# Kernel tuning notes

Hardware: AMD Instinct MI355X
Metric: run time of the kernel (lower is better)

Reference implementation:

```python
import jax, jax.numpy as jnp
import numpy as np

N = 8192        # nodes
E = 49152       # edges (~avg degree 6, triangular mesh)
H = 6           # GATv2 heads
C = 512         # hidden_size (per-head out channels)
F_IN = 2 + C    # GATv2 in_channels = coord(2) + hidden(512)
ALL_FEAT = 37   # deform_in_c-2 + 16 + 16
NUM_LOOP = 3
LRELU_SLOPE = 0.2


def setup_inputs() -> dict:
    key = jax.random.key(0)
    ks = jax.random.split(key, 10)
    x = jax.random.uniform(ks[0], (N, 7), dtype=jnp.float32)
    local_feat = jax.random.normal(ks[1], (N, 16), dtype=jnp.float32)
    conv_feat = jax.random.normal(ks[2], (N, 16), dtype=jnp.float32)
    edge_index = jax.random.randint(ks[3], (2, E), 0, N, dtype=jnp.int64)
    bd_mask = jnp.zeros((N,), jnp.int32)  # poly_mesh=False path
    W_lin = jax.random.normal(ks[4], (ALL_FEAT, C), dtype=jnp.float32) / np.float32(np.sqrt(ALL_FEAT))
    b_lin = jnp.zeros((C,), jnp.float32)
    Wl = jax.random.normal(ks[5], (F_IN, H * C), dtype=jnp.float32) / np.float32(np.sqrt(F_IN))
    Wr = jax.random.normal(ks[6], (F_IN, H * C), dtype=jnp.float32) / np.float32(np.sqrt(F_IN))
    att = jax.random.normal(ks[7], (H, C), dtype=jnp.float32) / np.float32(np.sqrt(C))
    gat_bias = jnp.zeros((C,), jnp.float32)
    W_coord = jax.random.normal(ks[8], (C, 2), dtype=jnp.float32) / np.float32(np.sqrt(C))
    b_coord = jnp.zeros((2,), jnp.float32)
    return dict(x=x, local_feat=local_feat, conv_feat=conv_feat,
                W_lin=W_lin, b_lin=b_lin, Wl=Wl, Wr=Wr, att=att,
                gat_bias=gat_bias, W_coord=W_coord, b_coord=b_coord,
                edge_index=edge_index, bd_mask=bd_mask)


def _gatv2(feat, src, dst, Wl, Wr, att, bias):
    # PyG GATv2Conv: lin_l on source, lin_r on target, additive attention
    n = feat.shape[0]
    xl = (feat @ Wl).reshape(n, H, C)            # source-side transform
    xr = (feat @ Wr).reshape(n, H, C)            # target-side transform
    e = xl[src] + xr[dst]                        # [E', H, C]
    e = jax.nn.leaky_relu(e, LRELU_SLOPE)
    logits = jnp.einsum('ehc,hc->eh', e, att)    # [E', H]
    m = jax.ops.segment_max(logits, dst, num_segments=n)
    m = jnp.where(jnp.isfinite(m), m, 0.0)
    a = jnp.exp(logits - m[dst])
    denom = jax.ops.segment_sum(a, dst, num_segments=n) + 1e-16
    alpha = a / denom[dst]                       # segment softmax over incoming edges
    msg = xl[src] * alpha[:, :, None]            # [E', H, C]
    out = jax.ops.segment_sum(msg, dst, num_segments=n)  # [N, H, C]
    return out.mean(axis=1) + bias               # concat=False -> mean over heads


def reference(x, local_feat, conv_feat, W_lin, b_lin, Wl, Wr, att, gat_bias,
              W_coord, b_coord, edge_index, bd_mask):
    coord = x[:, :2]
    hidden_in = jnp.concatenate([x[:, 2:], local_feat, conv_feat], axis=1)
    hidden = jax.nn.selu(hidden_in @ W_lin + b_lin)
    # GATv2Conv adds self-loops by default
    loops = jnp.arange(N, dtype=edge_index.dtype)
    src = jnp.concatenate([edge_index[0], loops])
    dst = jnp.concatenate([edge_index[1], loops])
    for _ in range(NUM_LOOP):
        up = coord[:, 0] == 1.0
        down = coord[:, 0] == 0.0
        left = coord[:, 1] == 0.0
        right = coord[:, 1] == 1.0
        feat = jnp.concatenate([coord, hidden], axis=1)   # [N, 514]
        hidden = jax.nn.selu(_gatv2(feat, src, dst, Wl, Wr, att, gat_bias))
        out = hidden @ W_coord + b_coord                  # [N, 2]
        ox = jnp.where(down, 0.0, jnp.where(up, 1.0, out[:, 0]))
        oy = jnp.where(right, 1.0, jnp.where(left, 0.0, out[:, 1]))
        coord = jnp.stack([ox, oy], axis=1)
    return coord
```

## Files before the change

kernel.cpp:

```cpp
#include <hip/hip_runtime.h>
#include <hip/hip_bf16.h>
#include <math.h>

#define N_NODES   8192
#define NUM_E     49152
#define NUM_EDGES (NUM_E + N_NODES)
#define H_HEADS   6
#define C_DIM     512
#define HC        (H_HEADS * C_DIM)
#define XLR       (2 * HC)
#define N_FEAT    37
#define LRELU_SLOPE 0.2f
#define SELU_LAMBDA 1.0507009873554805f
#define SELU_ALPHA  1.6732632423543772f

typedef __bf16 bf16_t;
typedef bf16_t bf16x8 __attribute__((ext_vector_type(8)));
typedef bf16_t bf16x4 __attribute__((ext_vector_type(4)));
typedef float  f32x4  __attribute__((ext_vector_type(4)));
typedef float  f32x2  __attribute__((ext_vector_type(2)));

__device__ __forceinline__ int edge_src(const int* ei, int e) {
    return e < NUM_E ? ei[e] : (e - NUM_E);
}
__device__ __forceinline__ int edge_dst(const int* ei, int e) {
    return e < NUM_E ? ei[NUM_E + e] : (e - NUM_E);
}
__device__ __forceinline__ float selu_f(float v) {
    return v > 0.f ? SELU_LAMBDA * v : SELU_LAMBDA * SELU_ALPHA * (__expf(v) - 1.f);
}
__device__ __forceinline__ void gload_lds16(const void* g, void* l) {
    __builtin_amdgcn_global_load_lds((const __attribute__((address_space(1))) void*)g,
                                     (__attribute__((address_space(3))) void*)l, 16, 0, 0);
}

__global__ __launch_bounds__(512) void k_hidden0(
    const float* __restrict__ x, const float* __restrict__ lf,
    const float* __restrict__ cf, const float* __restrict__ W,
    const float* __restrict__ b, bf16_t* __restrict__ hidden,
    float* __restrict__ coord)
{
    int n = blockIdx.x;
    int c = threadIdx.x;
    __shared__ float f[N_FEAT];
    if (c < 5)            f[c] = x[n*7 + 2 + c];
    else if (c < 21)      f[c] = lf[n*16 + (c-5)];
    else if (c < N_FEAT)  f[c] = cf[n*16 + (c-21)];
    if (c < 2) coord[n*2 + c] = x[n*7 + c];
    __syncthreads();
    float acc = b[c];
    #pragma unroll
    for (int k = 0; k < N_FEAT; ++k) acc = fmaf(f[k], W[k*C_DIM + c], acc);
    hidden[n*C_DIM + c] = (bf16_t)selu_f(acc);
}

__global__ __launch_bounds__(256) void k_wt_transpose(const float* __restrict__ W,
                                                      bf16_t* __restrict__ WT)
{
    __shared__ float tile[32][33];
    int k0 = blockIdx.y * 32;
    int n0 = blockIdx.x * 32;
    int tx = threadIdx.x & 31, ty = threadIdx.x >> 5;
    #pragma unroll
    for (int i = 0; i < 4; ++i)
        tile[ty + i*8][tx] = W[(size_t)(k0 + 2 + ty + i*8) * HC + n0 + tx];
    __syncthreads();
    #pragma unroll
    for (int i = 0; i < 4; ++i)
        WT[(size_t)(n0 + ty + i*8) * C_DIM + k0 + tx] = (bf16_t)tile[tx][ty + i*8];
}

__global__ void k_hist(const int* __restrict__ ei, int* __restrict__ counts) {
    int e = blockIdx.x * blockDim.x + threadIdx.x;
    if (e >= NUM_EDGES) return;
    atomicAdd(&counts[edge_dst(ei, e)], 1);
}

__global__ __launch_bounds__(256) void k_scan(const int* __restrict__ counts,
                                              int* __restrict__ row_ptr,
                                              int* __restrict__ cursor) {
    __shared__ int part[256];
    __shared__ int off[257];
    int t = threadIdx.x;
    int base = t * 32;
    int local[32];
    int s = 0;
    #pragma unroll
    for (int i = 0; i < 32; ++i) { local[i] = s; s += counts[base + i]; }
    part[t] = s;
    __syncthreads();
    if (t == 0) {
        off[0] = 0;
        for (int i = 0; i < 256; ++i) off[i+1] = off[i] + part[i];
    }
    __syncthreads();
    int o = off[t];
    #pragma unroll
    for (int i = 0; i < 32; ++i) {
        int v = o + local[i];
        row_ptr[base + i] = v;
        cursor[base + i]  = v;
    }
    if (t == 255) row_ptr[N_NODES] = off[256];
}

__global__ void k_scatter(const int* __restrict__ ei, int* __restrict__ cursor,
                          int* __restrict__ csr_src) {
    int e = blockIdx.x * blockDim.x + threadIdx.x;
    if (e >= NUM_EDGES) return;
    int pos = atomicAdd(&cursor[edge_dst(ei, e)], 1);
    csr_src[pos] = edge_src(ei, e);
}

#define GM 128
#define GN 128
#define GK 32
__global__ __launch_bounds__(256) void k_gemm_bf16(
    const bf16_t* __restrict__ A,
    const bf16_t* __restrict__ BT,
    const float*  __restrict__ Wl,
    const float*  __restrict__ Wr,
    const float*  __restrict__ coord,
    bf16_t* __restrict__ out)
{
    __shared__ bf16_t As[2][GM][GK];
    __shared__ bf16_t Bs[2][GM][GK];
    int tid  = threadIdx.x;
    int wave = tid >> 6;
    int lane = tid & 63;
    int rowBase = blockIdx.y * GM;
    int colBase = blockIdx.x * GN;
    int wr = (wave >> 1) * 64;
    int wc = (wave & 1) * 64;

    f32x4 acc[4][4] = {};

    int gsw = (((lane & 3) ^ ((lane >> 3) & 3))) * 8;
    const bf16_t* Ag = A  + (size_t)(rowBase + wave*32 + (lane >> 2)) * C_DIM + gsw;
    const bf16_t* Bg = BT + (size_t)(colBase + wave*32 + (lane >> 2)) * C_DIM + gsw;
    int m16 = lane & 15;
    int q8s = (((lane >> 4) ^ ((lane >> 1) & 3))) * 8;

    gload_lds16(Ag,            &As[0][wave*32     ][0]);
    gload_lds16(Ag + 16*C_DIM, &As[0][wave*32 + 16][0]);
    gload_lds16(Bg,            &Bs[0][wave*32     ][0]);
    gload_lds16(Bg + 16*C_DIM, &Bs[0][wave*32 + 16][0]);

    int p = 0;
    for (int k0 = 0; k0 < C_DIM; k0 += GK) {
        __syncthreads();
        if (k0 + GK < C_DIM) {
            gload_lds16(Ag + k0 + GK,            &As[p^1][wave*32     ][0]);
            gload_lds16(Ag + k0 + GK + 16*C_DIM, &As[p^1][wave*32 + 16][0]);
            gload_lds16(Bg + k0 + GK,            &Bs[p^1][wave*32     ][0]);
            gload_lds16(Bg + k0 + GK + 16*C_DIM, &Bs[p^1][wave*32 + 16][0]);
        }
        bf16x8 af[4], bfr[4];
        #pragma unroll
        for (int i = 0; i < 4; ++i) af[i]  = *(const bf16x8*)&As[p][wr + i*16 + m16][q8s];
        #pragma unroll
        for (int j = 0; j < 4; ++j) bfr[j] = *(const bf16x8*)&Bs[p][wc + j*16 + m16][q8s];
        #pragma unroll
        for (int i = 0; i < 4; ++i)
            #pragma unroll
            for (int j = 0; j < 4; ++j)
                acc[i][j] = __builtin_amdgcn_mfma_f32_16x16x32_bf16(bfr[j], af[i], acc[i][j], 0, 0, 0);
        p ^= 1;
    }

    const float* Wtop = (colBase < HC) ? Wl : Wr;
    int coff = (colBase < HC) ? 0 : HC;
    int q4 = (lane >> 4) * 4;

    float4 w0[4], w1[4];
    #pragma unroll
    for (int j = 0; j < 4; ++j) {
        int wcol = colBase + wc + j*16 + q4 - coff;
        w0[j] = *(const float4*)&Wtop[wcol];
        w1[j] = *(const float4*)&Wtop[HC + wcol];
    }
    #pragma unroll
    for (int i = 0; i < 4; ++i) {
        int row = rowBase + wr + i*16 + m16;
        float c0 = coord[row*2 + 0], c1 = coord[row*2 + 1];
        size_t rb = (size_t)row * XLR;
        #pragma unroll
        for (int j = 0; j < 4; ++j) {
            int col = colBase + wc + j*16 + q4;
            bf16x4 pk;
            pk[0] = (bf16_t)(acc[i][j][0] + c0 * w0[j].x + c1 * w1[j].x);
            pk[1] = (bf16_t)(acc[i][j][1] + c0 * w0[j].y + c1 * w1[j].y);
            pk[2] = (bf16_t)(acc[i][j][2] + c0 * w0[j].z + c1 * w1[j].z);
            pk[3] = (bf16_t)(acc[i][j][3] + c0 * w0[j].w + c1 * w1[j].w);
            *(bf16x4*)(out + rb + col) = pk;
        }
    }
}

#define MAX_DEG 128
__global__ __launch_bounds__(384) void k_attn_agg(
    const bf16_t* __restrict__ xlr,
    const int* __restrict__ row_ptr, const int* __restrict__ csr_src,
    const float* __restrict__ att,
    const float* __restrict__ gat_bias, const float* __restrict__ W_coord,
    const float* __restrict__ b_coord, const float* __restrict__ coord_in,
    bf16_t* __restrict__ hidden, float* __restrict__ coord_out)
{
    int n = blockIdx.x;
    int tid = threadIdx.x;
    int h = tid >> 6, lane = tid & 63;
    __shared__ int   s_src[MAX_DEG];
    __shared__ float s_acc[HC];
    __shared__ float s_red[12];

    int beg = row_ptr[n];
    int deg = min(row_ptr[n + 1] - beg, MAX_DEG);
    for (int j = tid; j < deg; j += 384) s_src[j] = csr_src[beg + j];
    __syncthreads();

    size_t off = (size_t)h * C_DIM + lane * 8;
    bf16x8 xrv = *(const bf16x8*)(xlr + (size_t)n * XLR + HC + off);
    f32x2 xr2[4], at2[4], ac2[4] = {};
    #pragma unroll
    for (int i = 0; i < 4; ++i) {
        xr2[i] = f32x2{(float)xrv[2*i], (float)xrv[2*i+1]};
        at2[i] = f32x2{att[off + 2*i], att[off + 2*i + 1]};
    }

    float l = 0.f;
    int j = 0;
    for (; j + 2 <= deg; j += 2) {
        bf16x8 xa = *(const bf16x8*)(xlr + (size_t)s_src[j]     * XLR + off);
        bf16x8 xb = *(const bf16x8*)(xlr + (size_t)s_src[j + 1] * XLR + off);
        f32x2 xla[4], xlb[4];
        #pragma unroll
        for (int i = 0; i < 4; ++i) {
            xla[i] = f32x2{(float)xa[2*i], (float)xa[2*i+1]};
            xlb[i] = f32x2{(float)xb[2*i], (float)xb[2*i+1]};
        }
        f32x2 sa = {0.f, 0.f}, sb = {0.f, 0.f};
        #pragma unroll
        for (int i = 0; i < 4; ++i) {
            f32x2 va = xla[i] + xr2[i];
            f32x2 vb = xlb[i] + xr2[i];
            sa += __builtin_elementwise_max(va, va * LRELU_SLOPE) * at2[i];
            sb += __builtin_elementwise_max(vb, vb * LRELU_SLOPE) * at2[i];
        }
        float suma = sa.x + sa.y, sumb = sb.x + sb.y;
        #pragma unroll
        for (int o = 1; o < 64; o <<= 1) {
            suma += __shfl_xor(suma, o);
            sumb += __shfl_xor(sumb, o);
        }
        float aa = __expf(suma), ab = __expf(sumb);
        l += aa + ab;
        #pragma unroll
        for (int i = 0; i < 4; ++i) ac2[i] += aa * xla[i] + ab * xlb[i];
    }
    if (j < deg) {
        bf16x8 xa = *(const bf16x8*)(xlr + (size_t)s_src[j] * XLR + off);
        f32x2 xla[4];
        #pragma unroll
        for (int i = 0; i < 4; ++i) xla[i] = f32x2{(float)xa[2*i], (float)xa[2*i+1]};
        f32x2 sa = {0.f, 0.f};
        #pragma unroll
        for (int i = 0; i < 4; ++i) {
            f32x2 va = xla[i] + xr2[i];
            sa += __builtin_elementwise_max(va, va * LRELU_SLOPE) * at2[i];
        }
        float suma = sa.x + sa.y;
        #pragma unroll
        for (int o = 1; o < 64; o <<= 1) suma += __shfl_xor(suma, o);
        float aa = __expf(suma);
        l += aa;
        #pragma unroll
        for (int i = 0; i < 4; ++i) ac2[i] += aa * xla[i];
    }

    float invl = 1.f / (l + 1e-16f) * (1.f / 6.f);
    #pragma unroll
    for (int i = 0; i < 4; ++i) {
        s_acc[off + 2*i]     = ac2[i].x * invl;
        s_acc[off + 2*i + 1] = ac2[i].y * invl;
    }
    __syncthreads();

    float p0 = 0.f, p1 = 0.f;
    for (int c = tid; c < C_DIM; c += 384) {
        float s = 0.f;
        #pragma unroll
        for (int hh = 0; hh < H_HEADS; ++hh) s += s_acc[hh * C_DIM + c];
        float hv = selu_f(s + gat_bias[c]);
        hidden[n * C_DIM + c] = (bf16_t)hv;
        p0 = fmaf(hv, W_coord[c * 2 + 0], p0);
        p1 = fmaf(hv, W_coord[c * 2 + 1], p1);
    }
    #pragma unroll
    for (int o = 32; o > 0; o >>= 1) { p0 += __shfl_down(p0, o); p1 += __shfl_down(p1, o); }
    if (lane == 0) { s_red[h * 2] = p0; s_red[h * 2 + 1] = p1; }
    __syncthreads();
    if (tid == 0) {
        float o0 = b_coord[0], o1 = b_coord[1];
        #pragma unroll
        for (int w = 0; w < H_HEADS; ++w) { o0 += s_red[w * 2]; o1 += s_red[w * 2 + 1]; }
        float cx = coord_in[n * 2 + 0], cy = coord_in[n * 2 + 1];
        float ox = (cx == 0.0f) ? 0.f : ((cx == 1.0f) ? 1.f : o0);
        float oy = (cy == 1.0f) ? 1.f : ((cy == 0.0f) ? 0.f : o1);
        coord_out[n * 2 + 0] = ox;
        coord_out[n * 2 + 1] = oy;
    }
}

extern "C" void kernel_launch(void* const* d_in, const int* in_sizes, int n_in,
                              void* d_out, int out_size, void* d_ws, size_t ws_size,
                              hipStream_t stream)
{
    const float* x       = (const float*)d_in[0];
    const float* lf      = (const float*)d_in[1];
    const float* cf      = (const float*)d_in[2];
    const float* W_lin   = (const float*)d_in[3];
    const float* b_lin   = (const float*)d_in[4];
    const float* Wl      = (const float*)d_in[5];
    const float* Wr      = (const float*)d_in[6];
    const float* att     = (const float*)d_in[7];
    const float* gbias   = (const float*)d_in[8];
    const float* W_coord = (const float*)d_in[9];
    const float* b_coord = (const float*)d_in[10];
    const int*   ei      = (const int*)d_in[11];

    char* w = (char*)d_ws;
    auto alloc = [&](size_t bytes) { char* p = w; w += (bytes + 255) & ~255ull; return p; };
    bf16_t*   hidden  = (bf16_t*)alloc((size_t)N_NODES * C_DIM * 2);
    bf16_t*   WT      = (bf16_t*)alloc((size_t)XLR * C_DIM * 2);
    bf16_t*   xlr     = (bf16_t*)alloc((size_t)N_NODES * XLR * 2);
    int*      counts  = (int*)alloc((size_t)N_NODES * 4);
    int*      row_ptr = (int*)alloc((size_t)(N_NODES + 1) * 4);
    int*      cursor  = (int*)alloc((size_t)N_NODES * 4);
    int*      csr_src = (int*)alloc((size_t)NUM_EDGES * 4);
    float*    cA      = (float*)alloc((size_t)N_NODES * 2 * 4);
    float*    cB      = (float*)alloc((size_t)N_NODES * 2 * 4);

    hipMemsetAsync(counts, 0, (size_t)N_NODES * 4, stream);
    k_hidden0<<<N_NODES, 512, 0, stream>>>(x, lf, cf, W_lin, b_lin, hidden, cA);
    {
        dim3 tg(HC / 32, C_DIM / 32);
        k_wt_transpose<<<tg, 256, 0, stream>>>(Wl, WT);
        k_wt_transpose<<<tg, 256, 0, stream>>>(Wr, WT + (size_t)HC * C_DIM);
    }
    k_hist<<<(NUM_EDGES + 255) / 256, 256, 0, stream>>>(ei, counts);
    k_scan<<<1, 256, 0, stream>>>(counts, row_ptr, cursor);
    k_scatter<<<(NUM_EDGES + 255) / 256, 256, 0, stream>>>(ei, cursor, csr_src);

    float* cin = cA;
    for (int it = 0; it < 3; ++it) {
        float* cout = (it == 2) ? (float*)d_out : ((it == 0) ? cB : cA);
        dim3 g(XLR / GN, N_NODES / GM);
        k_gemm_bf16<<<g, 256, 0, stream>>>(hidden, WT, Wl, Wr, cin, xlr);
        k_attn_agg<<<N_NODES, 384, 0, stream>>>(xlr, row_ptr, csr_src, att,
                                                gbias, W_coord, b_coord, cin, hidden, cout);
        cin = cout;
    }
}
```

Before: 603.5 us.

## Load GEMM fragments directly from global memory, dropping LDS staging

```diff
diff --git a/kernel.cpp b/kernel.cpp
--- a/kernel.cpp
+++ b/kernel.cpp
@@ -29,10 +29,6 @@
 __device__ __forceinline__ float selu_f(float v) {
     return v > 0.f ? SELU_LAMBDA * v : SELU_LAMBDA * SELU_ALPHA * (__expf(v) - 1.f);
 }
-__device__ __forceinline__ void gload_lds16(const void* g, void* l) {
-    __builtin_amdgcn_global_load_lds((const __attribute__((address_space(1))) void*)g,
-                                     (__attribute__((address_space(3))) void*)l, 16, 0, 0);
-}
 
 __global__ __launch_bounds__(512) void k_hidden0(
     const float* __restrict__ x, const float* __restrict__ lf,
@@ -114,7 +110,6 @@
 
 #define GM 128
 #define GN 128
-#define GK 32
 __global__ __launch_bounds__(256) void k_gemm_bf16(
     const bf16_t* __restrict__ A,
     const bf16_t* __restrict__ BT,
@@ -123,75 +118,59 @@
     const float*  __restrict__ coord,
     bf16_t* __restrict__ out)
 {
-    __shared__ bf16_t As[2][GM][GK];
-    __shared__ bf16_t Bs[2][GM][GK];
     int tid  = threadIdx.x;
     int wave = tid >> 6;
     int lane = tid & 63;
-    int rowBase = blockIdx.y * GM;
-    int colBase = blockIdx.x * GN;
-    int wr = (wave >> 1) * 64;
-    int wc = (wave & 1) * 64;
+    int rowBase = blockIdx.y * GM + (wave >> 1) * 64;
+    int colBase = blockIdx.x * GN + (wave & 1) * 64;
+    int m16 = lane & 15;
+    int q8  = (lane >> 4) * 8;
+
+    const bf16_t* Ap[4];
+    const bf16_t* Bp[4];
+    #pragma unroll
+    for (int i = 0; i < 4; ++i) {
+        Ap[i] = A  + (size_t)(rowBase + i*16 + m16) * C_DIM + q8;
+        Bp[i] = BT + (size_t)(colBase + i*16 + m16) * C_DIM + q8;
+    }
 
     f32x4 acc[4][4] = {};
 
-    int gsw = (((lane & 3) ^ ((lane >> 3) & 3))) * 8;
-    const bf16_t* Ag = A  + (size_t)(rowBase + wave*32 + (lane >> 2)) * C_DIM + gsw;
-    const bf16_t* Bg = BT + (size_t)(colBase + wave*32 + (lane >> 2)) * C_DIM + gsw;
-    int m16 = lane & 15;
-    int q8s = (((lane >> 4) ^ ((lane >> 1) & 3))) * 8;
-
-    gload_lds16(Ag,            &As[0][wave*32     ][0]);
-    gload_lds16(Ag + 16*C_DIM, &As[0][wave*32 + 16][0]);
-    gload_lds16(Bg,            &Bs[0][wave*32     ][0]);
-    gload_lds16(Bg + 16*C_DIM, &Bs[0][wave*32 + 16][0]);
-
-    int p = 0;
-    for (int k0 = 0; k0 < C_DIM; k0 += GK) {
-        __syncthreads();
-        if (k0 + GK < C_DIM) {
-            gload_lds16(Ag + k0 + GK,            &As[p^1][wave*32     ][0]);
-            gload_lds16(Ag + k0 + GK + 16*C_DIM, &As[p^1][wave*32 + 16][0]);
-            gload_lds16(Bg + k0 + GK,            &Bs[p^1][wave*32     ][0]);
-            gload_lds16(Bg + k0 + GK + 16*C_DIM, &Bs[p^1][wave*32 + 16][0]);
-        }
+    #pragma unroll 2
+    for (int k0 = 0; k0 < C_DIM; k0 += 32) {
         bf16x8 af[4], bfr[4];
         #pragma unroll
-        for (int i = 0; i < 4; ++i) af[i]  = *(const bf16x8*)&As[p][wr + i*16 + m16][q8s];
-        #pragma unroll
-        for (int j = 0; j < 4; ++j) bfr[j] = *(const bf16x8*)&Bs[p][wc + j*16 + m16][q8s];
+        for (int i = 0; i < 4; ++i) af[i]  = *(const bf16x8*)(Ap[i] + k0);
+        #pragma unroll
+        for (int j = 0; j < 4; ++j) bfr[j] = *(const bf16x8*)(Bp[j] + k0);
         #pragma unroll
         for (int i = 0; i < 4; ++i)
             #pragma unroll
             for (int j = 0; j < 4; ++j)
                 acc[i][j] = __builtin_amdgcn_mfma_f32_16x16x32_bf16(bfr[j], af[i], acc[i][j], 0, 0, 0);
-        p ^= 1;
-    }
-
-    const float* Wtop = (colBase < HC) ? Wl : Wr;
-    int coff = (colBase < HC) ? 0 : HC;
+    }
+
+    int colB0 = blockIdx.x * GN;
+    const float* Wtop = (colB0 < HC) ? Wl : Wr;
+    int coff = (colB0 < HC) ? 0 : HC;
     int q4 = (lane >> 4) * 4;
 
-    float4 w0[4], w1[4];
-    #pragma unroll
-    for (int j = 0; j < 4; ++j) {
-        int wcol = colBase + wc + j*16 + q4 - coff;
-        w0[j] = *(const float4*)&Wtop[wcol];
-        w1[j] = *(const float4*)&Wtop[HC + wcol];
-    }
     #pragma unroll
     for (int i = 0; i < 4; ++i) {
-        int row = rowBase + wr + i*16 + m16;
+        int row = rowBase + i*16 + m16;
         float c0 = coord[row*2 + 0], c1 = coord[row*2 + 1];
         size_t rb = (size_t)row * XLR;
         #pragma unroll
         for (int j = 0; j < 4; ++j) {
-            int col = colBase + wc + j*16 + q4;
+            int col = colBase + j*16 + q4;
+            int wcol = col - coff;
+            float4 w0 = *(const float4*)&Wtop[wcol];
+            float4 w1 = *(const float4*)&Wtop[HC + wcol];
             bf16x4 pk;
-            pk[0] = (bf16_t)(acc[i][j][0] + c0 * w0[j].x + c1 * w1[j].x);
-            pk[1] = (bf16_t)(acc[i][j][1] + c0 * w0[j].y + c1 * w1[j].y);
-            pk[2] = (bf16_t)(acc[i][j][2] + c0 * w0[j].z + c1 * w1[j].z);
-            pk[3] = (bf16_t)(acc[i][j][3] + c0 * w0[j].w + c1 * w1[j].w);
+            pk[0] = (bf16_t)(acc[i][j][0] + c0 * w0.x + c1 * w1.x);
+            pk[1] = (bf16_t)(acc[i][j][1] + c0 * w0.y + c1 * w1.y);
+            pk[2] = (bf16_t)(acc[i][j][2] + c0 * w0.z + c1 * w1.z);
+            pk[3] = (bf16_t)(acc[i][j][3] + c0 * w0.w + c1 * w1.w);
             *(bf16x4*)(out + rb + col) = pk;
         }
     }
```

Result: slower. 959.4 us (+59.0%).

## Shrink GEMM tile to 128x64 with 2 waves, drop LDS double buffering

Applied to the files above, without the earlier changes.

```diff
diff --git a/kernel.cpp b/kernel.cpp
--- a/kernel.cpp
+++ b/kernel.cpp
@@ -113,9 +113,9 @@
 }
 
 #define GM 128
-#define GN 128
+#define GN 64
 #define GK 32
-__global__ __launch_bounds__(256) void k_gemm_bf16(
+__global__ __launch_bounds__(128, 5) void k_gemm_bf16(
     const bf16_t* __restrict__ A,
     const bf16_t* __restrict__ BT,
     const float*  __restrict__ Wl,
@@ -123,49 +123,42 @@
     const float*  __restrict__ coord,
     bf16_t* __restrict__ out)
 {
-    __shared__ bf16_t As[2][GM][GK];
-    __shared__ bf16_t Bs[2][GM][GK];
+    __shared__ bf16_t As[GM][GK];
+    __shared__ bf16_t Bs[GN][GK];
     int tid  = threadIdx.x;
     int wave = tid >> 6;
     int lane = tid & 63;
     int rowBase = blockIdx.y * GM;
     int colBase = blockIdx.x * GN;
-    int wr = (wave >> 1) * 64;
-    int wc = (wave & 1) * 64;
+    int wr = wave * 64;
 
     f32x4 acc[4][4] = {};
 
     int gsw = (((lane & 3) ^ ((lane >> 3) & 3))) * 8;
-    const bf16_t* Ag = A  + (size_t)(rowBase + wave*32 + (lane >> 2)) * C_DIM + gsw;
+    const bf16_t* Ag = A  + (size_t)(rowBase + wr + (lane >> 2)) * C_DIM + gsw;
     const bf16_t* Bg = BT + (size_t)(colBase + wave*32 + (lane >> 2)) * C_DIM + gsw;
     int m16 = lane & 15;
     int q8s = (((lane >> 4) ^ ((lane >> 1) & 3))) * 8;
 
-    gload_lds16(Ag,            &As[0][wave*32     ][0]);
-    gload_lds16(Ag + 16*C_DIM, &As[0][wave*32 + 16][0]);
-    gload_lds16(Bg,            &Bs[0][wave*32     ][0]);
-    gload_lds16(Bg + 16*C_DIM, &Bs[0][wave*32 + 16][0]);
-
-    int p = 0;
     for (int k0 = 0; k0 < C_DIM; k0 += GK) {
+        gload_lds16(Ag + k0,            &As[wr     ][0]);
+        gload_lds16(Ag + k0 + 16*C_DIM, &As[wr + 16][0]);
+        gload_lds16(Ag + k0 + 32*C_DIM, &As[wr + 32][0]);
+        gload_lds16(Ag + k0 + 48*C_DIM, &As[wr + 48][0]);
+        gload_lds16(Bg + k0,            &Bs[wave*32     ][0]);
+        gload_lds16(Bg + k0 + 16*C_DIM, &Bs[wave*32 + 16][0]);
         __syncthreads();
-        if (k0 + GK < C_DIM) {
-            gload_lds16(Ag + k0 + GK,            &As[p^1][wave*32     ][0]);
-            gload_lds16(Ag + k0 + GK + 16*C_DIM, &As[p^1][wave*32 + 16][0]);
-            gload_lds16(Bg + k0 + GK,            &Bs[p^1][wave*32     ][0]);
-            gload_lds16(Bg + k0 + GK + 16*C_DIM, &Bs[p^1][wave*32 + 16][0]);
-        }
         bf16x8 af[4], bfr[4];
         #pragma unroll
-        for (int i = 0; i < 4; ++i) af[i]  = *(const bf16x8*)&As[p][wr + i*16 + m16][q8s];
-        #pragma unroll
-        for (int j = 0; j < 4; ++j) bfr[j] = *(const bf16x8*)&Bs[p][wc + j*16 + m16][q8s];
+        for (int i = 0; i < 4; ++i) af[i]  = *(const bf16x8*)&As[wr + i*16 + m16][q8s];
+        #pragma unroll
+        for (int j = 0; j < 4; ++j) bfr[j] = *(const bf16x8*)&Bs[j*16 + m16][q8s];
         #pragma unroll
         for (int i = 0; i < 4; ++i)
             #pragma unroll
             for (int j = 0; j < 4; ++j)
                 acc[i][j] = __builtin_amdgcn_mfma_f32_16x16x32_bf16(bfr[j], af[i], acc[i][j], 0, 0, 0);
-        p ^= 1;
+        __syncthreads();
     }
 
     const float* Wtop = (colBase < HC) ? Wl : Wr;
@@ -175,7 +168,7 @@
     float4 w0[4], w1[4];
     #pragma unroll
     for (int j = 0; j < 4; ++j) {
-        int wcol = colBase + wc + j*16 + q4 - coff;
+        int wcol = colBase + j*16 + q4 - coff;
         w0[j] = *(const float4*)&Wtop[wcol];
         w1[j] = *(const float4*)&Wtop[HC + wcol];
     }
@@ -186,7 +179,7 @@
         size_t rb = (size_t)row * XLR;
         #pragma unroll
         for (int j = 0; j < 4; ++j) {
-            int col = colBase + wc + j*16 + q4;
+            int col = colBase + j*16 + q4;
             bf16x4 pk;
             pk[0] = (bf16_t)(acc[i][j][0] + c0 * w0[j].x + c1 * w1[j].x);
             pk[1] = (bf16_t)(acc[i][j][1] + c0 * w0[j].y + c1 * w1[j].y);
@@ -355,7 +348,7 @@
     for (int it = 0; it < 3; ++it) {
         float* cout = (it == 2) ? (float*)d_out : ((it == 0) ? cB : cA);
         dim3 g(XLR / GN, N_NODES / GM);
-        k_gemm_bf16<<<g, 256, 0, stream>>>(hidden, WT, Wl, Wr, cin, xlr);
+        k_gemm_bf16<<<g, 128, 0, stream>>>(hidden, WT, Wl, Wr, cin, xlr);
         k_attn_agg<<<N_NODES, 384, 0, stream>>>(xlr, row_ptr, csr_src, att,
                                                 gbias, W_coord, b_coord, cin, hidden, cout);
         cin = cout;
```

After: 740.4 us. 1.23x slower.
